# Performance work log

Measured on AMD Instinct MI355X. Metric: run time of the kernel, lower is better.

Reference implementation:

```python
import jax, jax.numpy as jnp
import numpy as np

N, D, B = 50000, 256, 2048
SIGMA = 1.0
SIGMA2 = SIGMA * SIGMA  # module stores np.square(sigma)


def setup_inputs() -> dict:
    key = jax.random.key(0)
    k1, k2, k3, k4 = jax.random.split(key, 4)
    x = jax.random.normal(k1, (B, D), dtype=jnp.float32)
    data_set = jax.random.normal(k2, (N, D), dtype=jnp.float32)
    # labels are +/-1
    data_labels = jnp.where(jax.random.uniform(k3, (N,)) < 0.5, -1.0, 1.0).astype(jnp.float32)
    # lambdas initialized to ones in the module; use small positive noise around 1/n scale
    lambdas = jax.random.uniform(k4, (N,), dtype=jnp.float32) * (2.0 / N)
    b = jnp.ones((1,), dtype=jnp.float32)
    return {"x": x, "data_set": data_set, "data_labels": data_labels,
            "lambdas": lambdas, "b": b}


def reference(x, data_set, data_labels, lambdas, b):
    x2 = jnp.sum(x * x, axis=1, keepdims=True)            # [B,1]
    s2 = jnp.sum(data_set * data_set, axis=1)             # [N]
    cross = jnp.einsum('bd,nd->bn', x, data_set)          # [B,N]
    sqdist = x2 + s2[None, :] - 2.0 * cross               # [B,N]
    K = jnp.exp(-sqdist / (2.0 * SIGMA2))                 # rbf kernel [B,N]
    w = data_labels * jax.nn.relu(lambdas)                # [N]
    return jnp.tanh(K @ w + b)                            # [B]
```

## Files before the change

kernel.cpp:

```cpp
#include <hip/hip_runtime.h>
#include <hip/hip_bf16.h>

#define NPTS 50000
#define DIM  256
#define BQ   2048
#define NPAD 50048

#define TILE 128
#define BK   32
#define NCHUNKS 391
#define NGROUPS 32
#define LOG2E 1.4426950408889634f

#define WS_ACC 0
#define WS_X2  2048
#define WS_S2  4096
#define WS_W   54144
#define WS_XB  104192
#define WS_SB  366336
#define WS_TOTAL_BYTES (6772480ull * 4ull)

#define V1_ACC 0
#define V1_X2  2048
#define V1_S2  4096
#define V1_W   54096

typedef __bf16 bf16x8 __attribute__((ext_vector_type(8)));
typedef __bf16 bf16x4 __attribute__((ext_vector_type(4)));
typedef float  f32x4  __attribute__((ext_vector_type(4)));
typedef unsigned int u32;

__device__ __forceinline__ float fast_exp2(float v) {
#if __has_builtin(__builtin_amdgcn_exp2f)
  return __builtin_amdgcn_exp2f(v);
#else
  return exp2f(v);
#endif
}

__device__ __forceinline__ void async_copy16(const __bf16* g, __bf16* l) {
  __builtin_amdgcn_global_load_lds(
      (const __attribute__((address_space(1))) u32*)g,
      (__attribute__((address_space(3))) u32*)l, 16, 0, 0);
}


__global__ __launch_bounds__(256) void svm_precvt4(
    const float* __restrict__ x, const float* __restrict__ s,
    const float* __restrict__ labels, const float* __restrict__ lambdas,
    float* __restrict__ ws) {
  const int wid  = blockIdx.x * 4 + (threadIdx.x >> 6);
  const int lane = threadIdx.x & 63;
  __bf16* xb = (__bf16*)(ws + WS_XB);
  __bf16* sb = (__bf16*)(ws + WS_SB);

  if (blockIdx.x < 8) ws[WS_ACC + blockIdx.x * 256 + threadIdx.x] = 0.0f;

  if (wid < NPAD) {
    float4 v = make_float4(0.f, 0.f, 0.f, 0.f);
    if (wid < NPTS)
      v = reinterpret_cast<const float4*>(s + (size_t)wid * DIM)[lane];
    bf16x4 h = { (__bf16)v.x, (__bf16)v.y, (__bf16)v.z, (__bf16)v.w };
    *reinterpret_cast<bf16x4*>(sb + (size_t)wid * DIM + lane * 4) = h;
    float ss = v.x * v.x + v.y * v.y + v.z * v.z + v.w * v.w;
    #pragma unroll
    for (int off = 32; off > 0; off >>= 1) ss += __shfl_xor(ss, off);
    if (lane == 0) {
      ws[WS_S2 + wid] = 0.5f * LOG2E * ss;
      float lam = (wid < NPTS) ? lambdas[wid] : 0.0f;
      float lab = (wid < NPTS) ? labels[wid] : 0.0f;
      ws[WS_W + wid] = lab * (lam > 0.0f ? lam : 0.0f);
    }
  } else if (wid < NPAD + BQ) {
    int r = wid - NPAD;
    float4 v = reinterpret_cast<const float4*>(x + (size_t)r * DIM)[lane];
    bf16x4 h = { (__bf16)v.x, (__bf16)v.y, (__bf16)v.z, (__bf16)v.w };
    *reinterpret_cast<bf16x4*>(xb + (size_t)r * DIM + lane * 4) = h;
    float ss = v.x * v.x + v.y * v.y + v.z * v.z + v.w * v.w;
    #pragma unroll
    for (int off = 32; off > 0; off >>= 1) ss += __shfl_xor(ss, off);
    if (lane == 0) ws[WS_X2 + r] = 0.5f * LOG2E * ss;
  }
}

__global__ __launch_bounds__(256, 2) void svm_main6(float* __restrict__ ws) {
  __shared__ __bf16 sB[8 * 128 * 32];

  const __bf16* xb = (const __bf16*)(ws + WS_XB);
  const __bf16* sb = (const __bf16*)(ws + WS_SB);
  const float* x2g = ws + WS_X2;
  const float* s2g = ws + WS_S2;
  const float* wg  = ws + WS_W;
  float* accOut    = ws + WS_ACC;

  const int t    = threadIdx.x;
  const int wave = t >> 6;
  const int lane = t & 63;
  const int quad = lane >> 4;
  const int l16  = lane & 15;
  const int bid  = blockIdx.x;
  const int g    = bid & 31;
  const int mt   = bid >> 5;
  const int m0   = mt * TILE;
  const int c0   = g * 12 + (g < 7 ? g : 7);
  const int cnt  = 12 + (g < 7 ? 1 : 0);

  f32x4 afr[2][8];
  #pragma unroll
  for (int mi = 0; mi < 2; ++mi)
    #pragma unroll
    for (int kt = 0; kt < 8; ++kt)
      afr[mi][kt] = *reinterpret_cast<const f32x4*>(
          xb + (size_t)(m0 + wave * 32 + mi * 16 + l16) * DIM + kt * BK + quad * 8);
  #pragma unroll
  for (int mi = 0; mi < 2; ++mi)
    #pragma unroll
    for (int kt = 0; kt < 8; ++kt)
      asm volatile("" : "+v"(afr[mi][kt]));

  float x2r[2][4];
  #pragma unroll
  for (int mi = 0; mi < 2; ++mi)
    #pragma unroll
    for (int r = 0; r < 4; ++r)
      x2r[mi][r] = x2g[m0 + wave * 32 + mi * 16 + quad * 4 + r];

  float runAcc[2][4] = {{0.f, 0.f, 0.f, 0.f}, {0.f, 0.f, 0.f, 0.f}};

  const int srcswz = ((lane & 3) ^ ((lane >> 3) & 3)) * 8;
  const int rdswz = (quad ^ ((l16 >> 1) & 3)) * 8;

  for (int c = c0; c < c0 + cnt; ++c) {
    __syncthreads();

    float s2t[8], wvv[8];
    #pragma unroll
    for (int ni = 0; ni < 8; ++ni) {
      int n = c * TILE + ni * 16 + l16;
      s2t[ni] = s2g[n];
      wvv[ni] = wg[n];
    }

    #pragma unroll
    for (int i = 0; i < 16; ++i) {
      int chunk = wave * 16 + i;
      int kt = chunk >> 3;
      int nb = (chunk & 7) * 16;
      const __bf16* src = sb + (size_t)(c * TILE + nb + (lane >> 2)) * DIM
                             + kt * BK + srcswz;
      async_copy16(src, &sB[kt * 4096 + nb * BK] + lane * 8);
    }
    __syncthreads();

    f32x4 acc[2][8];
    #pragma unroll
    for (int mi = 0; mi < 2; ++mi)
      #pragma unroll
      for (int ni = 0; ni < 8; ++ni)
        acc[mi][ni] = (f32x4)(0.0f);

    #pragma unroll
    for (int kt = 0; kt < 8; ++kt) {
      bf16x8 bfv[8];
      #pragma unroll
      for (int ni = 0; ni < 8; ++ni)
        bfv[ni] = *reinterpret_cast<const bf16x8*>(
            &sB[kt * 4096 + (ni * 16 + l16) * BK + rdswz]);
      #pragma unroll
      for (int mi = 0; mi < 2; ++mi)
        #pragma unroll
        for (int ni = 0; ni < 8; ++ni)
          acc[mi][ni] = __builtin_amdgcn_mfma_f32_16x16x32_bf16(
              __builtin_bit_cast(bf16x8, afr[mi][kt]), bfv[ni],
              acc[mi][ni], 0, 0, 0);
    }

    #pragma unroll
    for (int mi = 0; mi < 2; ++mi)
      #pragma unroll
      for (int reg = 0; reg < 4; ++reg) {
        float xh = x2r[mi][reg];
        float p = 0.0f;
        #pragma unroll
        for (int ni = 0; ni < 8; ++ni)
          p += fast_exp2(__builtin_fmaf(acc[mi][ni][reg], LOG2E,
                                        -(xh + s2t[ni]))) * wvv[ni];
        runAcc[mi][reg] += p;
      }
  }

  #pragma unroll
  for (int mi = 0; mi < 2; ++mi)
    #pragma unroll
    for (int reg = 0; reg < 4; ++reg) {
      float v = runAcc[mi][reg];
      v += __shfl_xor(v, 1);
      v += __shfl_xor(v, 2);
      v += __shfl_xor(v, 4);
      v += __shfl_xor(v, 8);
      if (l16 == 0)
        atomicAdd(&accOut[m0 + wave * 32 + mi * 16 + quad * 4 + reg], v);
    }
}


__global__ __launch_bounds__(256) void svm_precompute(
    const float* __restrict__ x, const float* __restrict__ s,
    const float* __restrict__ labels, const float* __restrict__ lambdas,
    float* __restrict__ ws) {
  int wid  = blockIdx.x * 4 + (threadIdx.x >> 6);
  int lane = threadIdx.x & 63;
  const float* src;
  if (wid < NPTS)           src = s + (size_t)wid * DIM;
  else if (wid < NPTS + BQ) src = x + (size_t)(wid - NPTS) * DIM;
  else return;
  float4 v = reinterpret_cast<const float4*>(src)[lane];
  float ss = v.x * v.x + v.y * v.y + v.z * v.z + v.w * v.w;
  #pragma unroll
  for (int off = 32; off > 0; off >>= 1) ss += __shfl_xor(ss, off);
  if (lane == 0) {
    if (wid < NPTS) {
      ws[V1_S2 + wid] = ss;
      float lam = lambdas[wid];
      ws[V1_W + wid] = labels[wid] * (lam > 0.0f ? lam : 0.0f);
    } else {
      ws[V1_X2 + (wid - NPTS)] = ss;
    }
  }
}

__global__ __launch_bounds__(256) void svm_main(
    const float* __restrict__ x, const float* __restrict__ s,
    const float* __restrict__ ws) {
  __shared__ __bf16 sA[128 * BK];
  __shared__ __bf16 sB[128 * BK];

  const int t    = threadIdx.x;
  const int wave = t >> 6;
  const int lane = t & 63;
  const int quad = lane >> 4;
  const int l16  = lane & 15;
  const int wm   = (wave & 1) * 64;
  const int wn   = (wave >> 1) * 64;
  const int bRow0 = blockIdx.y * 128;
  const int n0    = blockIdx.x * 128;

  f32x4 acc[4][4];
  #pragma unroll
  for (int i = 0; i < 4; ++i)
    #pragma unroll
    for (int j = 0; j < 4; ++j)
      acc[i][j] = (f32x4)(0.0f);

  for (int kt = 0; kt < DIM / BK; ++kt) {
    const int k0 = kt * BK;
    __syncthreads();
    #pragma unroll
    for (int i = 0; i < 4; ++i) {
      int slot = t + i * 256;
      int r  = slot >> 3;
      int c4 = slot & 7;
      float4 va = reinterpret_cast<const float4*>(
          x + (size_t)(bRow0 + r) * DIM + k0)[c4];
      bf16x4 ha = { (__bf16)va.x, (__bf16)va.y, (__bf16)va.z, (__bf16)va.w };
      *reinterpret_cast<bf16x4*>(&sA[r * BK + c4 * 4]) = ha;

      int nrow = n0 + r;
      float4 vb = make_float4(0.f, 0.f, 0.f, 0.f);
      if (nrow < NPTS)
        vb = reinterpret_cast<const float4*>(
            s + (size_t)nrow * DIM + k0)[c4];
      bf16x4 hb = { (__bf16)vb.x, (__bf16)vb.y, (__bf16)vb.z, (__bf16)vb.w };
      *reinterpret_cast<bf16x4*>(&sB[r * BK + c4 * 4]) = hb;
    }
    __syncthreads();

    bf16x8 af[4], bfv[4];
    #pragma unroll
    for (int mi = 0; mi < 4; ++mi)
      af[mi] = *reinterpret_cast<const bf16x8*>(
          &sA[(wm + mi * 16 + l16) * BK + quad * 8]);
    #pragma unroll
    for (int ni = 0; ni < 4; ++ni)
      bfv[ni] = *reinterpret_cast<const bf16x8*>(
          &sB[(wn + ni * 16 + l16) * BK + quad * 8]);
    #pragma unroll
    for (int mi = 0; mi < 4; ++mi)
      #pragma unroll
      for (int ni = 0; ni < 4; ++ni)
        acc[mi][ni] = __builtin_amdgcn_mfma_f32_16x16x32_bf16(
            af[mi], bfv[ni], acc[mi][ni], 0, 0, 0);
  }

  const float* x2g = ws + V1_X2;
  const float* s2g = ws + V1_S2;
  const float* wg  = ws + V1_W;
  float* accOut    = (float*)ws + V1_ACC;

  float s2v[4], wv[4];
  #pragma unroll
  for (int ni = 0; ni < 4; ++ni) {
    int n = n0 + wn + ni * 16 + l16;
    bool ok = n < NPTS;
    s2v[ni] = ok ? s2g[n] : 0.0f;
    wv[ni]  = ok ? wg[n]  : 0.0f;
  }
  #pragma unroll
  for (int mi = 0; mi < 4; ++mi) {
    const int mbase = wm + mi * 16 + quad * 4;
    #pragma unroll
    for (int reg = 0; reg < 4; ++reg) {
      float x2r = x2g[bRow0 + mbase + reg];
      float ps = 0.0f;
      #pragma unroll
      for (int ni = 0; ni < 4; ++ni) {
        float cc = acc[mi][ni][reg];
        ps += __expf(__builtin_fmaf(-0.5f, x2r + s2v[ni], cc)) * wv[ni];
      }
      ps += __shfl_xor(ps, 1);
      ps += __shfl_xor(ps, 2);
      ps += __shfl_xor(ps, 4);
      ps += __shfl_xor(ps, 8);
      if (l16 == 0) atomicAdd(&accOut[bRow0 + mbase + reg], ps);
    }
  }
}


__global__ __launch_bounds__(256) void svm_finalize(
    const float* __restrict__ ws, const float* __restrict__ bias,
    float* __restrict__ out) {
  int i = blockIdx.x * 256 + threadIdx.x;
  if (i < BQ) out[i] = tanhf(ws[i] + bias[0]);
}

extern "C" void kernel_launch(void* const* d_in, const int* in_sizes, int n_in,
                              void* d_out, int out_size, void* d_ws, size_t ws_size,
                              hipStream_t stream) {
  const float* x       = (const float*)d_in[0];
  const float* s       = (const float*)d_in[1];
  const float* labels  = (const float*)d_in[2];
  const float* lambdas = (const float*)d_in[3];
  const float* bias    = (const float*)d_in[4];
  float* out = (float*)d_out;
  float* ws  = (float*)d_ws;

  if (ws_size >= WS_TOTAL_BYTES) {
    svm_precvt4<<<(NPAD + BQ + 3) / 4, 256, 0, stream>>>(x, s, labels, lambdas, ws);
    svm_main6<<<16 * NGROUPS, 256, 0, stream>>>(ws);
  } else {
    hipMemsetAsync(ws, 0, BQ * sizeof(float), stream);
    svm_precompute<<<(NPTS + BQ + 3) / 4, 256, 0, stream>>>(x, s, labels, lambdas, ws);
    dim3 grid(391, BQ / 128);
    svm_main<<<grid, 256, 0, stream>>>(x, s, ws);
  }
  svm_finalize<<<BQ / 256, 256, 0, stream>>>(ws, bias, out);
}
```

Baseline: 159.3 us.

## Retile RBF-SVM main kernel to 256-row query tiles with 64-point chunks

Measured after the change: 183.0 us. 1.15x slower.

```diff
diff --git a/kernel.cpp b/kernel.cpp
--- a/kernel.cpp
+++ b/kernel.cpp
@@ -6,11 +6,12 @@
 #define BQ   2048
 #define NPAD 50048
 
-#define TILE 128
 #define BK   32
-#define NCHUNKS 391
-#define NGROUPS 32
 #define LOG2E 1.4426950408889634f
+
+#define CH    64
+#define NCH   782
+#define NGRP  64
 
 #define WS_ACC 0
 #define WS_X2  2048
@@ -83,8 +84,8 @@
   }
 }
 
-__global__ __launch_bounds__(256, 2) void svm_main6(float* __restrict__ ws) {
-  __shared__ __bf16 sB[8 * 128 * 32];
+__global__ __launch_bounds__(256, 2) void svm_main7(float* __restrict__ ws) {
+  __shared__ __bf16 sB[8 * CH * 32];
 
   const __bf16* xb = (const __bf16*)(ws + WS_XB);
   const __bf16* sb = (const __bf16*)(ws + WS_SB);
@@ -98,99 +99,95 @@
   const int lane = t & 63;
   const int quad = lane >> 4;
   const int l16  = lane & 15;
-  const int bid  = blockIdx.x;
-  const int g    = bid & 31;
-  const int mt   = bid >> 5;
-  const int m0   = mt * TILE;
-  const int c0   = g * 12 + (g < 7 ? g : 7);
-  const int cnt  = 12 + (g < 7 ? 1 : 0);
-
-  f32x4 afr[2][8];
-  #pragma unroll
-  for (int mi = 0; mi < 2; ++mi)
+  const int g    = blockIdx.x & 63;
+  const int mt   = blockIdx.x >> 6;
+  const int m0w  = mt * 256 + wave * 64;
+  const int c0   = (NCH * g) >> 6;
+  const int c1   = (NCH * (g + 1)) >> 6;
+
+  f32x4 afr[4][8];
+  #pragma unroll
+  for (int mi = 0; mi < 4; ++mi)
     #pragma unroll
     for (int kt = 0; kt < 8; ++kt)
       afr[mi][kt] = *reinterpret_cast<const f32x4*>(
-          xb + (size_t)(m0 + wave * 32 + mi * 16 + l16) * DIM + kt * BK + quad * 8);
-  #pragma unroll
-  for (int mi = 0; mi < 2; ++mi)
+          xb + (size_t)(m0w + mi * 16 + l16) * DIM + kt * BK + quad * 8);
+  #pragma unroll
+  for (int mi = 0; mi < 4; ++mi)
     #pragma unroll
     for (int kt = 0; kt < 8; ++kt)
       asm volatile("" : "+v"(afr[mi][kt]));
 
-  float x2r[2][4];
-  #pragma unroll
-  for (int mi = 0; mi < 2; ++mi)
-    #pragma unroll
-    for (int r = 0; r < 4; ++r)
-      x2r[mi][r] = x2g[m0 + wave * 32 + mi * 16 + quad * 4 + r];
-
-  float runAcc[2][4] = {{0.f, 0.f, 0.f, 0.f}, {0.f, 0.f, 0.f, 0.f}};
+  float runAcc[4][4];
+  #pragma unroll
+  for (int mi = 0; mi < 4; ++mi)
+    #pragma unroll
+    for (int r = 0; r < 4; ++r) runAcc[mi][r] = 0.0f;
 
   const int srcswz = ((lane & 3) ^ ((lane >> 3) & 3)) * 8;
   const int rdswz = (quad ^ ((l16 >> 1) & 3)) * 8;
 
-  for (int c = c0; c < c0 + cnt; ++c) {
+  for (int c = c0; c < c1; ++c) {
     __syncthreads();
 
-    float s2t[8], wvv[8];
-    #pragma unroll
-    for (int ni = 0; ni < 8; ++ni) {
-      int n = c * TILE + ni * 16 + l16;
-      s2t[ni] = s2g[n];
-      wvv[ni] = wg[n];
-    }
-
-    #pragma unroll
-    for (int i = 0; i < 16; ++i) {
-      int chunk = wave * 16 + i;
-      int kt = chunk >> 3;
-      int nb = (chunk & 7) * 16;
-      const __bf16* src = sb + (size_t)(c * TILE + nb + (lane >> 2)) * DIM
+    #pragma unroll
+    for (int i = 0; i < 8; ++i) {
+      int ch = wave * 8 + i;
+      int kt = ch >> 2;
+      int nb = (ch & 3) * 16;
+      const __bf16* src = sb + (size_t)(c * CH + nb + (lane >> 2)) * DIM
                              + kt * BK + srcswz;
-      async_copy16(src, &sB[kt * 4096 + nb * BK] + lane * 8);
+      async_copy16(src, &sB[kt * (CH * 32) + nb * 32] + lane * 8);
     }
     __syncthreads();
 
-    f32x4 acc[2][8];
-    #pragma unroll
-    for (int mi = 0; mi < 2; ++mi)
-      #pragma unroll
-      for (int ni = 0; ni < 8; ++ni)
+    f32x4 acc[4][4];
+    #pragma unroll
+    for (int mi = 0; mi < 4; ++mi)
+      #pragma unroll
+      for (int ni = 0; ni < 4; ++ni)
         acc[mi][ni] = (f32x4)(0.0f);
 
     #pragma unroll
     for (int kt = 0; kt < 8; ++kt) {
-      bf16x8 bfv[8];
-      #pragma unroll
-      for (int ni = 0; ni < 8; ++ni)
+      bf16x8 bfv[4];
+      #pragma unroll
+      for (int ni = 0; ni < 4; ++ni)
         bfv[ni] = *reinterpret_cast<const bf16x8*>(
-            &sB[kt * 4096 + (ni * 16 + l16) * BK + rdswz]);
-      #pragma unroll
-      for (int mi = 0; mi < 2; ++mi)
+            &sB[kt * (CH * 32) + (ni * 16 + l16) * 32 + rdswz]);
+      #pragma unroll
+      for (int mi = 0; mi < 4; ++mi)
         #pragma unroll
-        for (int ni = 0; ni < 8; ++ni)
+        for (int ni = 0; ni < 4; ++ni)
           acc[mi][ni] = __builtin_amdgcn_mfma_f32_16x16x32_bf16(
               __builtin_bit_cast(bf16x8, afr[mi][kt]), bfv[ni],
               acc[mi][ni], 0, 0, 0);
     }
 
-    #pragma unroll
-    for (int mi = 0; mi < 2; ++mi)
+    float s2t[4], wvv[4];
+    #pragma unroll
+    for (int ni = 0; ni < 4; ++ni) {
+      int n = c * CH + ni * 16 + l16;
+      s2t[ni] = s2g[n];
+      wvv[ni] = wg[n];
+    }
+    #pragma unroll
+    for (int mi = 0; mi < 4; ++mi) {
+      f32x4 xh = *reinterpret_cast<const f32x4*>(&x2g[m0w + mi * 16 + quad * 4]);
       #pragma unroll
       for (int reg = 0; reg < 4; ++reg) {
-        float xh = x2r[mi][reg];
         float p = 0.0f;
         #pragma unroll
-        for (int ni = 0; ni < 8; ++ni)
+        for (int ni = 0; ni < 4; ++ni)
           p += fast_exp2(__builtin_fmaf(acc[mi][ni][reg], LOG2E,
-                                        -(xh + s2t[ni]))) * wvv[ni];
+                                        -(xh[reg] + s2t[ni]))) * wvv[ni];
         runAcc[mi][reg] += p;
       }
-  }
-
-  #pragma unroll
-  for (int mi = 0; mi < 2; ++mi)
+    }
+  }
+
+  #pragma unroll
+  for (int mi = 0; mi < 4; ++mi)
     #pragma unroll
     for (int reg = 0; reg < 4; ++reg) {
       float v = runAcc[mi][reg];
@@ -199,7 +196,7 @@
       v += __shfl_xor(v, 4);
       v += __shfl_xor(v, 8);
       if (l16 == 0)
-        atomicAdd(&accOut[m0 + wave * 32 + mi * 16 + quad * 4 + reg], v);
+        atomicAdd(&accOut[m0w + mi * 16 + quad * 4 + reg], v);
     }
 }
 
@@ -233,7 +230,7 @@
     const float* __restrict__ x, const float* __restrict__ s,
     const float* __restrict__ ws) {
   __shared__ __bf16 sA[128 * BK];
-  __shared__ __bf16 sB[128 * BK];
+  __shared__ __bf16 sB2[128 * BK];
 
   const int t    = threadIdx.x;
   const int wave = t >> 6;
@@ -271,7 +268,7 @@
         vb = reinterpret_cast<const float4*>(
             s + (size_t)nrow * DIM + k0)[c4];
       bf16x4 hb = { (__bf16)vb.x, (__bf16)vb.y, (__bf16)vb.z, (__bf16)vb.w };
-      *reinterpret_cast<bf16x4*>(&sB[r * BK + c4 * 4]) = hb;
+      *reinterpret_cast<bf16x4*>(&sB2[r * BK + c4 * 4]) = hb;
     }
     __syncthreads();
 
@@ -283,7 +280,7 @@
     #pragma unroll
     for (int ni = 0; ni < 4; ++ni)
       bfv[ni] = *reinterpret_cast<const bf16x8*>(
-          &sB[(wn + ni * 16 + l16) * BK + quad * 8]);
+          &sB2[(wn + ni * 16 + l16) * BK + quad * 8]);
     #pragma unroll
     for (int mi = 0; mi < 4; ++mi)
       #pragma unroll
@@ -347,7 +344,7 @@
 
   if (ws_size >= WS_TOTAL_BYTES) {
     svm_precvt4<<<(NPAD + BQ + 3) / 4, 256, 0, stream>>>(x, s, labels, lambdas, ws);
-    svm_main6<<<16 * NGROUPS, 256, 0, stream>>>(ws);
+    svm_main7<<<8 * NGRP, 256, 0, stream>>>(ws);
   } else {
     hipMemsetAsync(ws, 0, BQ * sizeof(float), stream);
     svm_precompute<<<(NPTS + BQ + 3) / 4, 256, 0, stream>>>(x, s, labels, lambdas, ws);
```
